# Kernel optimization log

Hardware: AMD Instinct MI355X
Metric: run time of the kernel (lower is better)

Reference implementation:

```python
import jax, jax.numpy as jnp
import numpy as np

D_MODEL = 1024
NUM_HEADS = 16
HEAD_SIZE = D_MODEL // NUM_HEADS  # 64; used ONLY as the softmax scale (module never splits heads)


def setup_inputs() -> dict:
    key = jax.random.key(0)
    ks = jax.random.split(key, 7)
    B, L, D = 4, 2048, D_MODEL
    q = jax.random.normal(ks[0], (B, L, D), dtype=jnp.float32)
    k = jax.random.normal(ks[1], (B, L, D), dtype=jnp.float32)
    v = jax.random.normal(ks[2], (B, L, D), dtype=jnp.float32)
    s = 1.0 / np.sqrt(D)
    Wq = jax.random.uniform(ks[3], (D, D), jnp.float32, -s, s)
    Wk = jax.random.uniform(ks[4], (D, D), jnp.float32, -s, s)
    Wv = jax.random.uniform(ks[5], (D, D), jnp.float32, -s, s)
    Wproj = jax.random.uniform(ks[6], (D, D), jnp.float32, -s, s)
    return {"q": q, "k": k, "v": v, "Wq": Wq, "Wk": Wk, "Wv": Wv, "Wproj": Wproj}


def reference(q, k, v, Wq, Wk, Wv, Wproj):
    # nn.Linear(x) = x @ W.T; weights stored [out, in]
    L = q.shape[1]
    qh = jnp.einsum('bld,ed->ble', q, Wq)
    kh = jnp.einsum('bld,ed->ble', k, Wk)
    vh = jnp.einsum('bld,ed->ble', v, Wv)
    # NOTE: module attends over the full d_model channel (no head split),
    # but scales by head_size ** -0.5 — faithful to the source.
    att = jnp.einsum('bqd,bkd->bqk', qh, kh) * (HEAD_SIZE ** -0.5)
    causal = jnp.tril(jnp.ones((L, L), dtype=bool))  # bias buffer
    att = jnp.where(causal, att, -jnp.inf)
    att = jax.nn.softmax(att, axis=-1)
    y = jnp.einsum('bqk,bkd->bqd', att, vh)
    y = jnp.einsum('bld,ed->ble', y, Wproj)
    return y
```

## Files before the change

### kernel.cpp

```cpp
#include <hip/hip_runtime.h>
#include <hip/hip_bf16.h>
#include <stdint.h>

typedef __bf16 bf16x8 __attribute__((ext_vector_type(8)));
typedef float  f32x4  __attribute__((ext_vector_type(4)));
typedef unsigned short ushort8v __attribute__((ext_vector_type(8)));

__device__ __forceinline__ unsigned short f2bf(float f) {
  unsigned int u = __float_as_uint(f);
  u += 0x7FFF + ((u >> 16) & 1);
  return (unsigned short)(u >> 16);
}

#define GLOAD_LDS(gptr, ldsptr)                                                     \
  __builtin_amdgcn_global_load_lds(                                                 \
      (const __attribute__((address_space(1))) unsigned int*)(gptr),                \
      (__attribute__((address_space(3))) unsigned int*)(ldsptr), 16, 0, 0)

#define BM 128
#define BN 128
#define BK 32

__global__ __launch_bounds__(256, 3) void gemm_bt(
    const unsigned short* __restrict__ A,
    const unsigned short* __restrict__ B,
    void* __restrict__ C,
    int M, int N, int K, int ntiles,
    long sAz, long sBz, long sCz,
    int mode, int tilemap, float scale)
{
  int mt, nt;
  const int orig = blockIdx.x;
  if (tilemap == 0) {
    const int nwg = gridDim.x;
    const int qq = nwg >> 3, rr = nwg & 7, xc = orig & 7, oo = orig >> 3;
    const int wg = (xc < rr ? xc * (qq + 1) : rr * (qq + 1) + (xc - rr) * qq) + oo;
    mt = wg / ntiles; nt = wg % ntiles;
  } else if (tilemap == 1) {
    mt = (int)((sqrtf(8.f * orig + 1.f) - 1.f) * 0.5f);
    int base = mt * (mt + 1) / 2;
    if (orig < base) { mt--; base = mt * (mt + 1) / 2; }
    else if (orig >= base + mt + 1) { mt++; base = mt * (mt + 1) / 2; }
    nt = orig - base;
  } else {
    const int c = orig & 15;
    mt = (c & 8) ? (15 - (c & 7)) : c;
    nt = orig >> 4;
  }
  const int z = blockIdx.y;
  const int emode = (mode == 3) ? (z == 2 ? 1 : 0) : mode;

  A += sAz * (long)z;
  B += sBz * (long)z;

  __shared__ __align__(16) unsigned short As[3][BM * BK];
  __shared__ __align__(16) unsigned short Bs[3][BN * BK];

  const int tid  = threadIdx.x;
  const int wave = tid >> 6;
  const int lane = tid & 63;
  const int wr = wave >> 1, wc = wave & 1;

  f32x4 acc[4][4];
#pragma unroll
  for (int i = 0; i < 4; ++i)
#pragma unroll
    for (int j = 0; j < 4; ++j) acc[i][j] = (f32x4){0.f, 0.f, 0.f, 0.f};

  int kiters = K / BK;
  if (tilemap == 2) { const int kl = (mt + 1) * (BM / BK); if (kl < kiters) kiters = kl; }

  const int r0 = tid >> 2, s0 = tid & 3;
  const int c0 = ((s0 ^ ((r0 >> 1) & 3)) << 3);
  const int r1 = r0 + 64;
  const int c1 = ((s0 ^ ((r1 >> 1) & 3)) << 3);
  const long aoff0 = (long)(mt * BM + r0) * K + c0;
  const long aoff1 = (long)(mt * BM + r1) * K + c1;
  const long boff0 = (long)(nt * BN + r0) * K + c0;
  const long boff1 = (long)(nt * BN + r1) * K + c1;
  const unsigned ldsw = wave * 1024;

#define STAGE(bi, k0)                                                     \
  do {                                                                    \
    GLOAD_LDS(A + aoff0 + (k0), (char*)&As[bi][0]    + ldsw);             \
    GLOAD_LDS(A + aoff1 + (k0), (char*)&As[bi][2048] + ldsw);             \
    GLOAD_LDS(B + boff0 + (k0), (char*)&Bs[bi][0]    + ldsw);             \
    GLOAD_LDS(B + boff1 + (k0), (char*)&Bs[bi][2048] + ldsw);             \
  } while (0)

  STAGE(0, 0);
  if (kiters > 1) STAGE(1, BK);

  int cur = 0;
  for (int kt = 0; kt < kiters; ++kt) {
    const int rem = kiters - 1 - kt;
    if (rem >= 2) {
      int sb = cur + 2; if (sb >= 3) sb -= 3;
      STAGE(sb, (kt + 2) * BK);
      asm volatile("s_waitcnt vmcnt(8)" ::: "memory");
    } else if (rem == 1) {
      asm volatile("s_waitcnt vmcnt(4)" ::: "memory");
    } else {
      asm volatile("s_waitcnt vmcnt(0)" ::: "memory");
    }
    __builtin_amdgcn_s_barrier();
    asm volatile("" ::: "memory");

    bf16x8 af[4], bfr[4];
#pragma unroll
    for (int i = 0; i < 4; ++i) {
      const int ar = wr * 64 + i * 16 + (lane & 15);
      const int as = ((lane >> 4) ^ ((ar >> 1) & 3)) << 3;
      af[i] = *(const bf16x8*)&As[cur][ar * BK + as];
      const int br = wc * 64 + i * 16 + (lane & 15);
      const int bs = ((lane >> 4) ^ ((br >> 1) & 3)) << 3;
      bfr[i] = *(const bf16x8*)&Bs[cur][br * BK + bs];
    }
#pragma unroll
    for (int mi = 0; mi < 4; ++mi)
#pragma unroll
      for (int ni = 0; ni < 4; ++ni)
        acc[mi][ni] = __builtin_amdgcn_mfma_f32_16x16x32_bf16(af[mi], bfr[ni], acc[mi][ni], 0, 0, 0);

    asm volatile("" ::: "memory");
    __builtin_amdgcn_s_barrier();
    cur = (cur == 2) ? 0 : cur + 1;
  }
#undef STAGE

  const int rb = mt * BM + wr * 64;
  const int cb = nt * BN + wc * 64;

  if (emode == 0) {
    unsigned short* Cb = (unsigned short*)C + sCz * (long)z;
#pragma unroll
    for (int mi = 0; mi < 4; ++mi)
#pragma unroll
      for (int ni = 0; ni < 4; ++ni) {
        const int row0 = rb + mi * 16 + ((lane >> 4) << 2);
        const int col  = cb + ni * 16 + (lane & 15);
#pragma unroll
        for (int j = 0; j < 4; ++j)
          Cb[(long)(row0 + j) * N + col] = f2bf(acc[mi][ni][j]);
      }
  } else if (emode == 1) {
    unsigned short* Cb = (unsigned short*)C + sCz * (long)z;
#pragma unroll
    for (int mi = 0; mi < 4; ++mi)
#pragma unroll
      for (int ni = 0; ni < 4; ++ni) {
        const int row0 = rb + mi * 16 + ((lane >> 4) << 2);
        const int col  = cb + ni * 16 + (lane & 15);
#pragma unroll
        for (int j = 0; j < 4; ++j) {
          const int row = row0 + j;
          const int b = row >> 11, l = row & 2047;
          Cb[((long)b * N + col) * 2048 + l] = f2bf(acc[mi][ni][j]);
        }
      }
  } else {
    float* Cf = (float*)C + sCz * (long)z;
#pragma unroll
    for (int mi = 0; mi < 4; ++mi)
#pragma unroll
      for (int ni = 0; ni < 4; ++ni) {
        const int row0 = rb + mi * 16 + ((lane >> 4) << 2);
        const int col  = cb + ni * 16 + (lane & 15);
#pragma unroll
        for (int j = 0; j < 4; ++j)
          Cf[(long)(row0 + j) * N + col] = acc[mi][ni][j] * scale;
      }
  }
}

__global__ __launch_bounds__(256) void softmax_causal(
    const float* __restrict__ S, unsigned short* __restrict__ P, int L)
{
  const int r = blockIdx.x;
  const int b = r >> 11, q = r & 2047;
  const float* srow = S + ((long)b * L + q) * L;
  unsigned short* prow = P + ((long)b * L + q) * L;
  const int len = q + 1;
  const int lenceil = ((q >> 7) + 1) << 7;
  const int tid = threadIdx.x, lane = tid & 63, wave = tid >> 6;
  const int base = tid * 8;
  const bool active = base < lenceil;
  __shared__ float red[8];

  float vv[8];
#pragma unroll
  for (int i = 0; i < 8; ++i) vv[i] = -3.4e38f;
  if (active) {
    float4 x0 = ((const float4*)srow)[tid * 2];
    float4 x1 = ((const float4*)srow)[tid * 2 + 1];
    vv[0] = x0.x; vv[1] = x0.y; vv[2] = x0.z; vv[3] = x0.w;
    vv[4] = x1.x; vv[5] = x1.y; vv[6] = x1.z; vv[7] = x1.w;
  }

  float m = -3.4e38f;
#pragma unroll
  for (int i = 0; i < 8; ++i) if (base + i < len) m = fmaxf(m, vv[i]);
#pragma unroll
  for (int o = 32; o; o >>= 1) m = fmaxf(m, __shfl_xor(m, o));
  if (lane == 0) red[wave] = m;
  __syncthreads();
  m = fmaxf(fmaxf(red[0], red[1]), fmaxf(red[2], red[3]));

  float p[8], s = 0.f;
#pragma unroll
  for (int i = 0; i < 8; ++i) {
    p[i] = (base + i < len) ? __expf(vv[i] - m) : 0.f;
    s += p[i];
  }
#pragma unroll
  for (int o = 32; o; o >>= 1) s += __shfl_xor(s, o);
  if (lane == 0) red[4 + wave] = s;
  __syncthreads();
  s = (red[4] + red[5]) + (red[6] + red[7]);
  const float inv = 1.f / s;

  if (active) {
    ushort8v o16;
#pragma unroll
    for (int i = 0; i < 8; ++i) o16[i] = f2bf(p[i] * inv);
    *(ushort8v*)(prow + base) = o16;
  }
}

__global__ __launch_bounds__(256) void convert_all(
    const float* __restrict__ q, const float* __restrict__ k, const float* __restrict__ v,
    const float* __restrict__ wq, const float* __restrict__ wk,
    const float* __restrict__ wv, const float* __restrict__ wp,
    unsigned short* __restrict__ qkv, unsigned short* __restrict__ wb)
{
  const long NQ = 8192L * 1024 / 4;
  const long NW = 1024L * 1024 / 4;
  const int blk = blockIdx.x;
  const float* src; unsigned short* dst; long n; int nb, bb;
  if (blk < 1536) {
    const int s = blk >> 9;
    src = (s == 0) ? q : (s == 1) ? k : v;
    dst = qkv + (long)s * (8192L * 1024);
    n = NQ; nb = 512; bb = blk & 511;
  } else {
    const int s = (blk - 1536) >> 6;
    src = (s == 0) ? wq : (s == 1) ? wk : (s == 2) ? wv : wp;
    dst = wb + (long)s * (1024L * 1024);
    n = NW; nb = 64; bb = (blk - 1536) & 63;
  }
  for (long i = (long)bb * 256 + threadIdx.x; i < n; i += (long)nb * 256) {
    float4 x = ((const float4*)src)[i];
    ushort4 o;
    o.x = f2bf(x.x); o.y = f2bf(x.y); o.z = f2bf(x.z); o.w = f2bf(x.w);
    ((ushort4*)dst)[i] = o;
  }
}

extern "C" void kernel_launch(void* const* d_in, const int* in_sizes, int n_in,
                              void* d_out, int out_size, void* d_ws, size_t ws_size,
                              hipStream_t stream) {
  const float* q  = (const float*)d_in[0];
  const float* k  = (const float*)d_in[1];
  const float* v  = (const float*)d_in[2];
  const float* Wq = (const float*)d_in[3];
  const float* Wk = (const float*)d_in[4];
  const float* Wv = (const float*)d_in[5];
  const float* Wp = (const float*)d_in[6];
  float* out = (float*)d_out;

  const long D  = 1024;
  const long L  = 2048;
  const long ND = 8192 * D;
  const long NS = 4L * L * L;

  char* ws = (char*)d_ws;
  unsigned short* qh    = (unsigned short*)ws;
  unsigned short* kh    = qh  + ND;
  unsigned short* vhT   = kh  + ND;
  unsigned short* P     = vhT + ND;
  unsigned short* ybf   = P   + NS;
  unsigned short* wbf   = ybf + ND;
  float*          S     = (float*)(wbf + 4L * D * D);
  unsigned short* qkvbf = (unsigned short*)S;

  convert_all<<<1792, 256, 0, stream>>>(q, k, v, Wq, Wk, Wv, Wp, qkvbf, wbf);

  gemm_bt<<<dim3(512, 3), 256, 0, stream>>>(qkvbf, wbf, qh,
      8192, 1024, 1024, 8, ND, D * D, ND, 3, 0, 1.0f);

  gemm_bt<<<dim3(136, 4), 256, 0, stream>>>(qh, kh, S,
      2048, 2048, 1024, 16, L * D, L * D, L * L, 2, 1, 0.125f);

  softmax_causal<<<8192, 256, 0, stream>>>(S, P, 2048);

  gemm_bt<<<dim3(128, 4), 256, 0, stream>>>(P, vhT, ybf,
      2048, 1024, 2048, 8, L * L, D * L, L * D, 0, 2, 1.0f);

  gemm_bt<<<dim3(512, 1), 256, 0, stream>>>(ybf, wbf + 3 * D * D, out,
      8192, 1024, 1024, 8, 0, 0, 0, 2, 0, 1.0f);
}
```

Baseline: 221.0 us.

## Fuse fp32-to-bf16 activation conversion into QKV projection and store scores as bf16

Adds a proj_fused GEMM kernel that loads fp32 q/k/v straight from global memory into registers, converts them to bf16, and writes them into swizzled LDS. This removes the separate activation conversion pass and its bf16 staging buffer, and a smaller convert_w kernel now converts only the weights. The QK^T GEMM now writes scaled scores as bf16 instead of fp32, which halves score traffic into softmax. The cost is reduced precision of pre-softmax logits, plus a register-staged A path with manual waitcnt pipelining that may stall more than direct global-to-LDS loads.

Result: no change. 223.2 us (+1.0%).

```diff
diff --git a/kernel.cpp b/kernel.cpp
--- a/kernel.cpp
+++ b/kernel.cpp
@@ -11,6 +11,9 @@
   u += 0x7FFF + ((u >> 16) & 1);
   return (unsigned short)(u >> 16);
 }
+__device__ __forceinline__ float bf2f(unsigned short h) {
+  return __uint_as_float(((unsigned int)h) << 16);
+}
 
 #define GLOAD_LDS(gptr, ldsptr)                                                     \
   __builtin_amdgcn_global_load_lds(                                                 \
@@ -20,6 +23,158 @@
 #define BM 128
 #define BN 128
 #define BK 32
+
+__global__ __launch_bounds__(256, 3) void proj_fused(
+    const float* __restrict__ Aq, const float* __restrict__ Ak, const float* __restrict__ Av,
+    const unsigned short* __restrict__ W,
+    unsigned short* __restrict__ Out)
+{
+  const int K = 1024, N = 1024;
+  const int nwg = gridDim.x, orig = blockIdx.x;
+  const int qq = nwg >> 3, rr = nwg & 7, xc = orig & 7, oo = orig >> 3;
+  const int wg = (xc < rr ? xc * (qq + 1) : rr * (qq + 1) + (xc - rr) * qq) + oo;
+  const int mt = wg >> 3, nt = wg & 7;
+  const int z = blockIdx.y;
+  const float* A = (z == 0) ? Aq : (z == 1) ? Ak : Av;
+  const unsigned short* B = W + (long)z * (1024 * 1024);
+
+  __shared__ __align__(16) unsigned short As[2][128 * 32];
+  __shared__ __align__(16) unsigned short Bs[3][128 * 32];
+
+  const int tid = threadIdx.x, wave = tid >> 6, lane = tid & 63;
+  const int wr = wave >> 1, wc = wave & 1;
+
+  f32x4 acc[4][4];
+#pragma unroll
+  for (int i = 0; i < 4; ++i)
+#pragma unroll
+    for (int j = 0; j < 4; ++j) acc[i][j] = (f32x4){0.f, 0.f, 0.f, 0.f};
+
+  const int arow = tid >> 1;
+  const int acs  = (tid & 1) * 2;
+  const int asw  = (arow >> 1) & 3;
+  const float* abase = A + (long)(mt * 128 + arow) * K + acs * 8;
+  unsigned short* wp00 = &As[0][arow * 32 + ((acs    ) ^ asw) * 8];
+  unsigned short* wp01 = &As[0][arow * 32 + ((acs + 1) ^ asw) * 8];
+  unsigned short* wp10 = &As[1][arow * 32 + ((acs    ) ^ asw) * 8];
+  unsigned short* wp11 = &As[1][arow * 32 + ((acs + 1) ^ asw) * 8];
+
+  const int r0 = tid >> 2, s0 = tid & 3;
+  const int c0 = ((s0 ^ ((r0 >> 1) & 3)) << 3);
+  const int r1 = r0 + 64;
+  const int c1 = ((s0 ^ ((r1 >> 1) & 3)) << 3);
+  const long boff0 = (long)(nt * 128 + r0) * K + c0;
+  const long boff1 = (long)(nt * 128 + r1) * K + c1;
+  const unsigned ldsw = wave * 1024;
+
+  float4 rAe0, rAe1, rAe2, rAe3, rAo0, rAo1, rAo2, rAo3;
+
+#define LOADAE(kt) do { const float4* p_ = (const float4*)(abase + (kt) * 32);      \
+    rAe0 = p_[0]; rAe1 = p_[1]; rAe2 = p_[2]; rAe3 = p_[3]; } while (0)
+#define LOADAO(kt) do { const float4* p_ = (const float4*)(abase + (kt) * 32);      \
+    rAo0 = p_[0]; rAo1 = p_[1]; rAo2 = p_[2]; rAo3 = p_[3]; } while (0)
+#define BSTAGE(m, kt) do {                                                          \
+    GLOAD_LDS(B + boff0 + (kt) * 32, (char*)&Bs[m][0]    + ldsw);                   \
+    GLOAD_LDS(B + boff1 + (kt) * 32, (char*)&Bs[m][2048] + ldsw); } while (0)
+#define CVTW(bi, a0, a1, a2, a3) do {                                               \
+    ushort8v h0_, h1_;                                                              \
+    h0_[0]=f2bf(a0.x); h0_[1]=f2bf(a0.y); h0_[2]=f2bf(a0.z); h0_[3]=f2bf(a0.w);     \
+    h0_[4]=f2bf(a1.x); h0_[5]=f2bf(a1.y); h0_[6]=f2bf(a1.z); h0_[7]=f2bf(a1.w);     \
+    h1_[0]=f2bf(a2.x); h1_[1]=f2bf(a2.y); h1_[2]=f2bf(a2.z); h1_[3]=f2bf(a2.w);     \
+    h1_[4]=f2bf(a3.x); h1_[5]=f2bf(a3.y); h1_[6]=f2bf(a3.z); h1_[7]=f2bf(a3.w);     \
+    if (bi) { *(ushort8v*)wp10 = h0_; *(ushort8v*)wp11 = h1_; }                     \
+    else    { *(ushort8v*)wp00 = h0_; *(ushort8v*)wp01 = h1_; } } while (0)
+#define COMPUTE(abuf, bmod) do {                                                    \
+    bf16x8 af_[4], bf_[4];                                                          \
+    _Pragma("unroll")                                                               \
+    for (int i_ = 0; i_ < 4; ++i_) {                                                \
+      const int ar_ = wr * 64 + i_ * 16 + (lane & 15);                              \
+      const int as_ = ((lane >> 4) ^ ((ar_ >> 1) & 3)) << 3;                        \
+      af_[i_] = *(const bf16x8*)&As[abuf][ar_ * 32 + as_];                          \
+      const int br_ = wc * 64 + i_ * 16 + (lane & 15);                              \
+      const int bs_ = ((lane >> 4) ^ ((br_ >> 1) & 3)) << 3;                        \
+      bf_[i_] = *(const bf16x8*)&Bs[bmod][br_ * 32 + bs_]; }                        \
+    _Pragma("unroll")                                                               \
+    for (int mi_ = 0; mi_ < 4; ++mi_)                                               \
+    _Pragma("unroll")                                                               \
+      for (int ni_ = 0; ni_ < 4; ++ni_)                                             \
+        acc[mi_][ni_] = __builtin_amdgcn_mfma_f32_16x16x32_bf16(                    \
+            af_[mi_], bf_[ni_], acc[mi_][ni_], 0, 0, 0); } while (0)
+
+  LOADAE(0); LOADAO(1);
+  BSTAGE(0, 0); BSTAGE(1, 1);
+  asm volatile("s_waitcnt vmcnt(2)" ::: "memory");
+  CVTW(0, rAe0, rAe1, rAe2, rAe3);
+  asm volatile("s_waitcnt lgkmcnt(0)" ::: "memory");
+  __builtin_amdgcn_s_barrier();
+  asm volatile("" ::: "memory");
+
+  int m0 = 0;
+  for (int kt = 0; kt < 30; kt += 2) {
+    const int m1 = (m0 + 1) % 3, m2 = (m0 + 2) % 3;
+    LOADAE(kt + 2);
+    BSTAGE(m2, kt + 2);
+    COMPUTE(0, m0);
+    asm volatile("s_waitcnt vmcnt(6)" ::: "memory");
+    CVTW(1, rAo0, rAo1, rAo2, rAo3);
+    asm volatile("s_waitcnt lgkmcnt(0)" ::: "memory");
+    __builtin_amdgcn_s_barrier();
+    asm volatile("" ::: "memory");
+    LOADAO(kt + 3);
+    BSTAGE(m0, kt + 3);
+    COMPUTE(1, m1);
+    asm volatile("s_waitcnt vmcnt(6)" ::: "memory");
+    CVTW(0, rAe0, rAe1, rAe2, rAe3);
+    asm volatile("s_waitcnt lgkmcnt(0)" ::: "memory");
+    __builtin_amdgcn_s_barrier();
+    asm volatile("" ::: "memory");
+    m0 = m2;
+  }
+  COMPUTE(0, 0);
+  asm volatile("s_waitcnt vmcnt(0)" ::: "memory");
+  CVTW(1, rAo0, rAo1, rAo2, rAo3);
+  asm volatile("s_waitcnt lgkmcnt(0)" ::: "memory");
+  __builtin_amdgcn_s_barrier();
+  asm volatile("" ::: "memory");
+  COMPUTE(1, 1);
+
+#undef LOADAE
+#undef LOADAO
+#undef BSTAGE
+#undef CVTW
+#undef COMPUTE
+
+  const int rb = mt * 128 + wr * 64;
+  const int cb = nt * 128 + wc * 64;
+  if (z < 2) {
+    unsigned short* Cb = Out + (long)z * (8192L * 1024);
+#pragma unroll
+    for (int mi = 0; mi < 4; ++mi)
+#pragma unroll
+      for (int ni = 0; ni < 4; ++ni) {
+        const int row0 = rb + mi * 16 + ((lane >> 4) << 2);
+        const int col  = cb + ni * 16 + (lane & 15);
+#pragma unroll
+        for (int j = 0; j < 4; ++j)
+          Cb[(long)(row0 + j) * N + col] = f2bf(acc[mi][ni][j]);
+      }
+  } else {
+    unsigned short* Cb = Out + 2L * (8192L * 1024);
+#pragma unroll
+    for (int mi = 0; mi < 4; ++mi)
+#pragma unroll
+      for (int ni = 0; ni < 4; ++ni) {
+        const int row0 = rb + mi * 16 + ((lane >> 4) << 2);
+        const int col  = cb + ni * 16 + (lane & 15);
+#pragma unroll
+        for (int j = 0; j < 4; ++j) {
+          const int row = row0 + j;
+          const int b = row >> 11, l = row & 2047;
+          Cb[((long)b * N + col) * 2048 + l] = f2bf(acc[mi][ni][j]);
+        }
+      }
+  }
+}
 
 __global__ __launch_bounds__(256, 3) void gemm_bt(
     const unsigned short* __restrict__ A,
@@ -48,7 +203,6 @@
     nt = orig >> 4;
   }
   const int z = blockIdx.y;
-  const int emode = (mode == 3) ? (z == 2 ? 1 : 0) : mode;
 
   A += sAz * (long)z;
   B += sBz * (long)z;
@@ -131,7 +285,7 @@
   const int rb = mt * BM + wr * 64;
   const int cb = nt * BN + wc * 64;
 
-  if (emode == 0) {
+  if (mode == 0) {
     unsigned short* Cb = (unsigned short*)C + sCz * (long)z;
 #pragma unroll
     for (int mi = 0; mi < 4; ++mi)
@@ -141,10 +295,10 @@
         const int col  = cb + ni * 16 + (lane & 15);
 #pragma unroll
         for (int j = 0; j < 4; ++j)
-          Cb[(long)(row0 + j) * N + col] = f2bf(acc[mi][ni][j]);
+          Cb[(long)(row0 + j) * N + col] = f2bf(acc[mi][ni][j] * scale);
       }
-  } else if (emode == 1) {
-    unsigned short* Cb = (unsigned short*)C + sCz * (long)z;
+  } else {
+    float* Cf = (float*)C + sCz * (long)z;
 #pragma unroll
     for (int mi = 0; mi < 4; ++mi)
 #pragma unroll
@@ -152,21 +306,6 @@
         const int row0 = rb + mi * 16 + ((lane >> 4) << 2);
         const int col  = cb + ni * 16 + (lane & 15);
 #pragma unroll
-        for (int j = 0; j < 4; ++j) {
-          const int row = row0 + j;
-          const int b = row >> 11, l = row & 2047;
-          Cb[((long)b * N + col) * 2048 + l] = f2bf(acc[mi][ni][j]);
-        }
-      }
-  } else {
-    float* Cf = (float*)C + sCz * (long)z;
-#pragma unroll
-    for (int mi = 0; mi < 4; ++mi)
-#pragma unroll
-      for (int ni = 0; ni < 4; ++ni) {
-        const int row0 = rb + mi * 16 + ((lane >> 4) << 2);
-        const int col  = cb + ni * 16 + (lane & 15);
-#pragma unroll
         for (int j = 0; j < 4; ++j)
           Cf[(long)(row0 + j) * N + col] = acc[mi][ni][j] * scale;
       }
@@ -174,12 +313,12 @@
 }
 
 __global__ __launch_bounds__(256) void softmax_causal(
-    const float* __restrict__ S, unsigned short* __restrict__ P, int L)
+    const unsigned short* __restrict__ S, unsigned short* __restrict__ P)
 {
   const int r = blockIdx.x;
   const int b = r >> 11, q = r & 2047;
-  const float* srow = S + ((long)b * L + q) * L;
-  unsigned short* prow = P + ((long)b * L + q) * L;
+  const unsigned short* srow = S + ((long)b * 2048 + q) * 2048;
+  unsigned short* prow = P + ((long)b * 2048 + q) * 2048;
   const int len = q + 1;
   const int lenceil = ((q >> 7) + 1) << 7;
   const int tid = threadIdx.x, lane = tid & 63, wave = tid >> 6;
@@ -191,10 +330,9 @@
 #pragma unroll
   for (int i = 0; i < 8; ++i) vv[i] = -3.4e38f;
   if (active) {
-    float4 x0 = ((const float4*)srow)[tid * 2];
-    float4 x1 = ((const float4*)srow)[tid * 2 + 1];
-    vv[0] = x0.x; vv[1] = x0.y; vv[2] = x0.z; vv[3] = x0.w;
-    vv[4] = x1.x; vv[5] = x1.y; vv[6] = x1.z; vv[7] = x1.w;
+    ushort8v xv = *(const ushort8v*)(srow + base);
+#pragma unroll
+    for (int i = 0; i < 8; ++i) vv[i] = bf2f(xv[i]);
   }
 
   float m = -3.4e38f;
@@ -227,32 +365,21 @@
   }
 }
 
-__global__ __launch_bounds__(256) void convert_all(
-    const float* __restrict__ q, const float* __restrict__ k, const float* __restrict__ v,
+__global__ __launch_bounds__(256) void convert_w(
     const float* __restrict__ wq, const float* __restrict__ wk,
     const float* __restrict__ wv, const float* __restrict__ wp,
-    unsigned short* __restrict__ qkv, unsigned short* __restrict__ wb)
+    unsigned short* __restrict__ wb)
 {
-  const long NQ = 8192L * 1024 / 4;
-  const long NW = 1024L * 1024 / 4;
-  const int blk = blockIdx.x;
-  const float* src; unsigned short* dst; long n; int nb, bb;
-  if (blk < 1536) {
-    const int s = blk >> 9;
-    src = (s == 0) ? q : (s == 1) ? k : v;
-    dst = qkv + (long)s * (8192L * 1024);
-    n = NQ; nb = 512; bb = blk & 511;
-  } else {
-    const int s = (blk - 1536) >> 6;
-    src = (s == 0) ? wq : (s == 1) ? wk : (s == 2) ? wv : wp;
-    dst = wb + (long)s * (1024L * 1024);
-    n = NW; nb = 64; bb = (blk - 1536) & 63;
-  }
-  for (long i = (long)bb * 256 + threadIdx.x; i < n; i += (long)nb * 256) {
-    float4 x = ((const float4*)src)[i];
+  const long NV = 262144;
+  for (long i = (long)blockIdx.x * 256 + threadIdx.x; i < 4 * NV;
+       i += (long)gridDim.x * 256) {
+    const int seg = (int)(i >> 18);
+    const long off = i & (NV - 1);
+    const float* src = (seg == 0) ? wq : (seg == 1) ? wk : (seg == 2) ? wv : wp;
+    float4 x = ((const float4*)src)[off];
     ushort4 o;
     o.x = f2bf(x.x); o.y = f2bf(x.y); o.z = f2bf(x.z); o.w = f2bf(x.w);
-    ((ushort4*)dst)[i] = o;
+    ((ushort4*)(wb + (long)seg * 1048576))[off] = o;
   }
 }
 
@@ -274,24 +401,22 @@
   const long NS = 4L * L * L;
 
   char* ws = (char*)d_ws;
-  unsigned short* qh    = (unsigned short*)ws;
-  unsigned short* kh    = qh  + ND;
-  unsigned short* vhT   = kh  + ND;
-  unsigned short* P     = vhT + ND;
-  unsigned short* ybf   = P   + NS;
-  unsigned short* wbf   = ybf + ND;
-  float*          S     = (float*)(wbf + 4L * D * D);
-  unsigned short* qkvbf = (unsigned short*)S;
-
-  convert_all<<<1792, 256, 0, stream>>>(q, k, v, Wq, Wk, Wv, Wp, qkvbf, wbf);
-
-  gemm_bt<<<dim3(512, 3), 256, 0, stream>>>(qkvbf, wbf, qh,
-      8192, 1024, 1024, 8, ND, D * D, ND, 3, 0, 1.0f);
+  unsigned short* qh  = (unsigned short*)ws;
+  unsigned short* kh  = qh  + ND;
+  unsigned short* vhT = kh  + ND;
+  unsigned short* P   = vhT + ND;
+  unsigned short* ybf = P   + NS;
+  unsigned short* wbf = ybf + ND;
+  unsigned short* S   = wbf + 4L * D * D;
+
+  convert_w<<<1024, 256, 0, stream>>>(Wq, Wk, Wv, Wp, wbf);
+
+  proj_fused<<<dim3(512, 3), 256, 0, stream>>>(q, k, v, wbf, qh);
 
   gemm_bt<<<dim3(136, 4), 256, 0, stream>>>(qh, kh, S,
-      2048, 2048, 1024, 16, L * D, L * D, L * L, 2, 1, 0.125f);
-
-  softmax_causal<<<8192, 256, 0, stream>>>(S, P, 2048);
+      2048, 2048, 1024, 16, L * D, L * D, L * L, 0, 1, 0.125f);
+
+  softmax_causal<<<8192, 256, 0, stream>>>(S, P);
 
   gemm_bt<<<dim3(128, 4), 256, 0, stream>>>(P, vhT, ybf,
       2048, 1024, 2048, 8, L * L, D * L, L * D, 0, 2, 1.0f);
```

## Store attention scores in bf16 and use 128x256 tiles for projection GEMMs

Applied to the files above, without the earlier changes.

The QK^T GEMM now writes scaled scores as bf16 instead of fp32, and the softmax kernel reads bf16. This halves the memory traffic of the large score matrix. A new gemm_wide kernel with 128x256 tiles and a triple-buffered LDS pipeline replaces gemm_bt for the QKV and output projections, raising reuse per block. The workspace layout is changed so that P aliases the converted-input buffer. Rounding the scores to bf16 before softmax loses some precision.

New measurement: 234.7 us. 1.06x slower.

```diff
diff --git a/kernel.cpp b/kernel.cpp
--- a/kernel.cpp
+++ b/kernel.cpp
@@ -11,11 +11,156 @@
   u += 0x7FFF + ((u >> 16) & 1);
   return (unsigned short)(u >> 16);
 }
+__device__ __forceinline__ float bf2f(unsigned short h) {
+  return __uint_as_float(((unsigned int)h) << 16);
+}
 
 #define GLOAD_LDS(gptr, ldsptr)                                                     \
   __builtin_amdgcn_global_load_lds(                                                 \
       (const __attribute__((address_space(1))) unsigned int*)(gptr),                \
       (__attribute__((address_space(3))) unsigned int*)(ldsptr), 16, 0, 0)
+
+__global__ __launch_bounds__(256, 2) void gemm_wide(
+    const unsigned short* __restrict__ A,
+    const unsigned short* __restrict__ B,
+    void* __restrict__ C,
+    int M, int N, int K, int ntiles,
+    long sAz, long sBz, long sCz,
+    int mode, float scale)
+{
+  const int nwg = gridDim.x, orig = blockIdx.x;
+  const int qq = nwg >> 3, rr = nwg & 7, xc = orig & 7, oo = orig >> 3;
+  const int wg = (xc < rr ? xc * (qq + 1) : rr * (qq + 1) + (xc - rr) * qq) + oo;
+  const int mt = wg / ntiles, nt = wg % ntiles;
+  const int z = blockIdx.y;
+  const int emode = (mode == 3) ? (z == 2 ? 1 : 0) : mode;
+
+  A += sAz * (long)z;
+  B += sBz * (long)z;
+
+  __shared__ __align__(16) unsigned short As[3][128 * 32];
+  __shared__ __align__(16) unsigned short Bs[3][256 * 32];
+
+  const int tid  = threadIdx.x;
+  const int wave = tid >> 6;
+  const int lane = tid & 63;
+  const int wr = wave >> 1, wc = wave & 1;
+
+  f32x4 acc[4][8];
+#pragma unroll
+  for (int i = 0; i < 4; ++i)
+#pragma unroll
+    for (int j = 0; j < 8; ++j) acc[i][j] = (f32x4){0.f, 0.f, 0.f, 0.f};
+
+  const int kiters = K / 32;
+
+  const int r0 = tid >> 2, s0 = tid & 3;
+  const int c0 = ((s0 ^ ((r0 >> 1) & 3)) << 3);
+  const long aoff0 = (long)(mt * 128 + r0) * K + c0;
+  const long aoff1 = (long)(mt * 128 + 64 + r0) * K + c0;
+  const long boff0 = (long)(nt * 256 + r0) * K + c0;
+  const long boff1 = (long)(nt * 256 + 64 + r0) * K + c0;
+  const long boff2 = (long)(nt * 256 + 128 + r0) * K + c0;
+  const long boff3 = (long)(nt * 256 + 192 + r0) * K + c0;
+  const unsigned ldsw = wave * 1024;
+
+#define STAGE(bi, k0)                                                     \
+  do {                                                                    \
+    GLOAD_LDS(A + aoff0 + (k0), (char*)&As[bi][0]    + ldsw);             \
+    GLOAD_LDS(A + aoff1 + (k0), (char*)&As[bi][2048] + ldsw);             \
+    GLOAD_LDS(B + boff0 + (k0), (char*)&Bs[bi][0]    + ldsw);             \
+    GLOAD_LDS(B + boff1 + (k0), (char*)&Bs[bi][2048] + ldsw);             \
+    GLOAD_LDS(B + boff2 + (k0), (char*)&Bs[bi][4096] + ldsw);             \
+    GLOAD_LDS(B + boff3 + (k0), (char*)&Bs[bi][6144] + ldsw);             \
+  } while (0)
+
+  STAGE(0, 0);
+  if (kiters > 1) STAGE(1, 32);
+
+  int cur = 0;
+  for (int kt = 0; kt < kiters; ++kt) {
+    const int rem = kiters - 1 - kt;
+    if (rem >= 2) {
+      int sb = cur + 2; if (sb >= 3) sb -= 3;
+      STAGE(sb, (kt + 2) * 32);
+      asm volatile("s_waitcnt vmcnt(12)" ::: "memory");
+    } else if (rem == 1) {
+      asm volatile("s_waitcnt vmcnt(6)" ::: "memory");
+    } else {
+      asm volatile("s_waitcnt vmcnt(0)" ::: "memory");
+    }
+    __builtin_amdgcn_s_barrier();
+    asm volatile("" ::: "memory");
+
+    bf16x8 af[4], bfr[8];
+#pragma unroll
+    for (int i = 0; i < 4; ++i) {
+      const int ar = wr * 64 + i * 16 + (lane & 15);
+      const int as = ((lane >> 4) ^ ((ar >> 1) & 3)) << 3;
+      af[i] = *(const bf16x8*)&As[cur][ar * 32 + as];
+    }
+#pragma unroll
+    for (int j = 0; j < 8; ++j) {
+      const int br = (j >> 2) * 128 + wc * 64 + (j & 3) * 16 + (lane & 15);
+      const int bs = ((lane >> 4) ^ ((br >> 1) & 3)) << 3;
+      bfr[j] = *(const bf16x8*)&Bs[cur][br * 32 + bs];
+    }
+#pragma unroll
+    for (int mi = 0; mi < 4; ++mi)
+#pragma unroll
+      for (int ni = 0; ni < 8; ++ni)
+        acc[mi][ni] = __builtin_amdgcn_mfma_f32_16x16x32_bf16(af[mi], bfr[ni], acc[mi][ni], 0, 0, 0);
+
+    asm volatile("" ::: "memory");
+    __builtin_amdgcn_s_barrier();
+    cur = (cur == 2) ? 0 : cur + 1;
+  }
+#undef STAGE
+
+  const int rb = mt * 128 + wr * 64;
+  const int cbase = nt * 256;
+
+  if (emode == 0) {
+    unsigned short* Cb = (unsigned short*)C + sCz * (long)z;
+#pragma unroll
+    for (int mi = 0; mi < 4; ++mi)
+#pragma unroll
+      for (int ni = 0; ni < 8; ++ni) {
+        const int row0 = rb + mi * 16 + ((lane >> 4) << 2);
+        const int col  = cbase + (ni >> 2) * 128 + wc * 64 + (ni & 3) * 16 + (lane & 15);
+#pragma unroll
+        for (int j = 0; j < 4; ++j)
+          Cb[(long)(row0 + j) * N + col] = f2bf(acc[mi][ni][j] * scale);
+      }
+  } else if (emode == 1) {
+    unsigned short* Cb = (unsigned short*)C + sCz * (long)z;
+#pragma unroll
+    for (int mi = 0; mi < 4; ++mi)
+#pragma unroll
+      for (int ni = 0; ni < 8; ++ni) {
+        const int row0 = rb + mi * 16 + ((lane >> 4) << 2);
+        const int col  = cbase + (ni >> 2) * 128 + wc * 64 + (ni & 3) * 16 + (lane & 15);
+#pragma unroll
+        for (int j = 0; j < 4; ++j) {
+          const int row = row0 + j;
+          const int b = row >> 11, l = row & 2047;
+          Cb[((long)b * N + col) * 2048 + l] = f2bf(acc[mi][ni][j]);
+        }
+      }
+  } else {
+    float* Cf = (float*)C + sCz * (long)z;
+#pragma unroll
+    for (int mi = 0; mi < 4; ++mi)
+#pragma unroll
+      for (int ni = 0; ni < 8; ++ni) {
+        const int row0 = rb + mi * 16 + ((lane >> 4) << 2);
+        const int col  = cbase + (ni >> 2) * 128 + wc * 64 + (ni & 3) * 16 + (lane & 15);
+#pragma unroll
+        for (int j = 0; j < 4; ++j)
+          Cf[(long)(row0 + j) * N + col] = acc[mi][ni][j] * scale;
+      }
+  }
+}
 
 #define BM 128
 #define BN 128
@@ -48,7 +193,6 @@
     nt = orig >> 4;
   }
   const int z = blockIdx.y;
-  const int emode = (mode == 3) ? (z == 2 ? 1 : 0) : mode;
 
   A += sAz * (long)z;
   B += sBz * (long)z;
@@ -131,7 +275,7 @@
   const int rb = mt * BM + wr * 64;
   const int cb = nt * BN + wc * 64;
 
-  if (emode == 0) {
+  if (mode == 0) {
     unsigned short* Cb = (unsigned short*)C + sCz * (long)z;
 #pragma unroll
     for (int mi = 0; mi < 4; ++mi)
@@ -141,10 +285,10 @@
         const int col  = cb + ni * 16 + (lane & 15);
 #pragma unroll
         for (int j = 0; j < 4; ++j)
-          Cb[(long)(row0 + j) * N + col] = f2bf(acc[mi][ni][j]);
+          Cb[(long)(row0 + j) * N + col] = f2bf(acc[mi][ni][j] * scale);
       }
-  } else if (emode == 1) {
-    unsigned short* Cb = (unsigned short*)C + sCz * (long)z;
+  } else {
+    float* Cf = (float*)C + sCz * (long)z;
 #pragma unroll
     for (int mi = 0; mi < 4; ++mi)
 #pragma unroll
@@ -152,21 +296,6 @@
         const int row0 = rb + mi * 16 + ((lane >> 4) << 2);
         const int col  = cb + ni * 16 + (lane & 15);
 #pragma unroll
-        for (int j = 0; j < 4; ++j) {
-          const int row = row0 + j;
-          const int b = row >> 11, l = row & 2047;
-          Cb[((long)b * N + col) * 2048 + l] = f2bf(acc[mi][ni][j]);
-        }
-      }
-  } else {
-    float* Cf = (float*)C + sCz * (long)z;
-#pragma unroll
-    for (int mi = 0; mi < 4; ++mi)
-#pragma unroll
-      for (int ni = 0; ni < 4; ++ni) {
-        const int row0 = rb + mi * 16 + ((lane >> 4) << 2);
-        const int col  = cb + ni * 16 + (lane & 15);
-#pragma unroll
         for (int j = 0; j < 4; ++j)
           Cf[(long)(row0 + j) * N + col] = acc[mi][ni][j] * scale;
       }
@@ -174,12 +303,12 @@
 }
 
 __global__ __launch_bounds__(256) void softmax_causal(
-    const float* __restrict__ S, unsigned short* __restrict__ P, int L)
+    const unsigned short* __restrict__ S, unsigned short* __restrict__ P)
 {
   const int r = blockIdx.x;
   const int b = r >> 11, q = r & 2047;
-  const float* srow = S + ((long)b * L + q) * L;
-  unsigned short* prow = P + ((long)b * L + q) * L;
+  const unsigned short* srow = S + ((long)b * 2048 + q) * 2048;
+  unsigned short* prow = P + ((long)b * 2048 + q) * 2048;
   const int len = q + 1;
   const int lenceil = ((q >> 7) + 1) << 7;
   const int tid = threadIdx.x, lane = tid & 63, wave = tid >> 6;
@@ -191,10 +320,9 @@
 #pragma unroll
   for (int i = 0; i < 8; ++i) vv[i] = -3.4e38f;
   if (active) {
-    float4 x0 = ((const float4*)srow)[tid * 2];
-    float4 x1 = ((const float4*)srow)[tid * 2 + 1];
-    vv[0] = x0.x; vv[1] = x0.y; vv[2] = x0.z; vv[3] = x0.w;
-    vv[4] = x1.x; vv[5] = x1.y; vv[6] = x1.z; vv[7] = x1.w;
+    ushort8v xv = *(const ushort8v*)(srow + base);
+#pragma unroll
+    for (int i = 0; i < 8; ++i) vv[i] = bf2f(xv[i]);
   }
 
   float m = -3.4e38f;
@@ -277,25 +405,25 @@
   unsigned short* qh    = (unsigned short*)ws;
   unsigned short* kh    = qh  + ND;
   unsigned short* vhT   = kh  + ND;
-  unsigned short* P     = vhT + ND;
-  unsigned short* ybf   = P   + NS;
-  unsigned short* wbf   = ybf + ND;
-  float*          S     = (float*)(wbf + 4L * D * D);
-  unsigned short* qkvbf = (unsigned short*)S;
+  unsigned short* wbf   = vhT + ND;
+  unsigned short* S     = wbf + 4L * D * D;
+  unsigned short* qkvbf = S   + NS;
+  unsigned short* P     = qkvbf;
+  unsigned short* ybf   = P + NS;
 
   convert_all<<<1792, 256, 0, stream>>>(q, k, v, Wq, Wk, Wv, Wp, qkvbf, wbf);
 
-  gemm_bt<<<dim3(512, 3), 256, 0, stream>>>(qkvbf, wbf, qh,
-      8192, 1024, 1024, 8, ND, D * D, ND, 3, 0, 1.0f);
+  gemm_wide<<<dim3(256, 3), 256, 0, stream>>>(qkvbf, wbf, qh,
+      8192, 1024, 1024, 4, ND, D * D, ND, 3, 1.0f);
 
   gemm_bt<<<dim3(136, 4), 256, 0, stream>>>(qh, kh, S,
-      2048, 2048, 1024, 16, L * D, L * D, L * L, 2, 1, 0.125f);
-
-  softmax_causal<<<8192, 256, 0, stream>>>(S, P, 2048);
+      2048, 2048, 1024, 16, L * D, L * D, L * L, 0, 1, 0.125f);
+
+  softmax_causal<<<8192, 256, 0, stream>>>(S, P);
 
   gemm_bt<<<dim3(128, 4), 256, 0, stream>>>(P, vhT, ybf,
       2048, 1024, 2048, 8, L * L, D * L, L * D, 0, 2, 1.0f);
 
-  gemm_bt<<<dim3(512, 1), 256, 0, stream>>>(ybf, wbf + 3 * D * D, out,
-      8192, 1024, 1024, 8, 0, 0, 0, 2, 0, 1.0f);
-}
+  gemm_wide<<<dim3(256, 1), 256, 0, stream>>>(ybf, wbf + 3 * D * D, out,
+      8192, 1024, 1024, 4, 0, 0, 0, 2, 1.0f);
+}
```

## Store attention scores in bf16 and switch GEMM to double-buffered LDS

Applied to the files above, without the earlier changes.

The QK^T GEMM now writes scaled scores as bf16 instead of fp32, and softmax reads them as bf16. This halves the score-matrix write and read traffic. Separately, the GEMM pipeline drops from three LDS stages to two, and launch bounds rise to allow more resident blocks per CU. Storing scores in bf16 loses precision before softmax. Shallower prefetch may expose more memory latency, traded for higher occupancy.

New measurement: 222.2 us. Within noise of the previous version (+0.5%).

```diff
diff --git a/kernel.cpp b/kernel.cpp
--- a/kernel.cpp
+++ b/kernel.cpp
@@ -11,6 +11,9 @@
   u += 0x7FFF + ((u >> 16) & 1);
   return (unsigned short)(u >> 16);
 }
+__device__ __forceinline__ float bf2f(unsigned short h) {
+  return __uint_as_float(((unsigned int)h) << 16);
+}
 
 #define GLOAD_LDS(gptr, ldsptr)                                                     \
   __builtin_amdgcn_global_load_lds(                                                 \
@@ -21,7 +24,7 @@
 #define BN 128
 #define BK 32
 
-__global__ __launch_bounds__(256, 3) void gemm_bt(
+__global__ __launch_bounds__(256, 5) void gemm_bt(
     const unsigned short* __restrict__ A,
     const unsigned short* __restrict__ B,
     void* __restrict__ C,
@@ -53,8 +56,8 @@
   A += sAz * (long)z;
   B += sBz * (long)z;
 
-  __shared__ __align__(16) unsigned short As[3][BM * BK];
-  __shared__ __align__(16) unsigned short Bs[3][BN * BK];
+  __shared__ __align__(16) unsigned short As[2][BM * BK];
+  __shared__ __align__(16) unsigned short Bs[2][BN * BK];
 
   const int tid  = threadIdx.x;
   const int wave = tid >> 6;
@@ -89,16 +92,11 @@
   } while (0)
 
   STAGE(0, 0);
-  if (kiters > 1) STAGE(1, BK);
 
   int cur = 0;
   for (int kt = 0; kt < kiters; ++kt) {
-    const int rem = kiters - 1 - kt;
-    if (rem >= 2) {
-      int sb = cur + 2; if (sb >= 3) sb -= 3;
-      STAGE(sb, (kt + 2) * BK);
-      asm volatile("s_waitcnt vmcnt(8)" ::: "memory");
-    } else if (rem == 1) {
+    if (kt + 1 < kiters) {
+      STAGE(cur ^ 1, (kt + 1) * BK);
       asm volatile("s_waitcnt vmcnt(4)" ::: "memory");
     } else {
       asm volatile("s_waitcnt vmcnt(0)" ::: "memory");
@@ -124,7 +122,7 @@
 
     asm volatile("" ::: "memory");
     __builtin_amdgcn_s_barrier();
-    cur = (cur == 2) ? 0 : cur + 1;
+    cur ^= 1;
   }
 #undef STAGE
 
@@ -141,7 +139,7 @@
         const int col  = cb + ni * 16 + (lane & 15);
 #pragma unroll
         for (int j = 0; j < 4; ++j)
-          Cb[(long)(row0 + j) * N + col] = f2bf(acc[mi][ni][j]);
+          Cb[(long)(row0 + j) * N + col] = f2bf(acc[mi][ni][j] * scale);
       }
   } else if (emode == 1) {
     unsigned short* Cb = (unsigned short*)C + sCz * (long)z;
@@ -174,12 +172,12 @@
 }
 
 __global__ __launch_bounds__(256) void softmax_causal(
-    const float* __restrict__ S, unsigned short* __restrict__ P, int L)
+    const unsigned short* __restrict__ S, unsigned short* __restrict__ P)
 {
   const int r = blockIdx.x;
   const int b = r >> 11, q = r & 2047;
-  const float* srow = S + ((long)b * L + q) * L;
-  unsigned short* prow = P + ((long)b * L + q) * L;
+  const unsigned short* srow = S + ((long)b * 2048 + q) * 2048;
+  unsigned short* prow = P + ((long)b * 2048 + q) * 2048;
   const int len = q + 1;
   const int lenceil = ((q >> 7) + 1) << 7;
   const int tid = threadIdx.x, lane = tid & 63, wave = tid >> 6;
@@ -191,10 +189,9 @@
 #pragma unroll
   for (int i = 0; i < 8; ++i) vv[i] = -3.4e38f;
   if (active) {
-    float4 x0 = ((const float4*)srow)[tid * 2];
-    float4 x1 = ((const float4*)srow)[tid * 2 + 1];
-    vv[0] = x0.x; vv[1] = x0.y; vv[2] = x0.z; vv[3] = x0.w;
-    vv[4] = x1.x; vv[5] = x1.y; vv[6] = x1.z; vv[7] = x1.w;
+    ushort8v xv = *(const ushort8v*)(srow + base);
+#pragma unroll
+    for (int i = 0; i < 8; ++i) vv[i] = bf2f(xv[i]);
   }
 
   float m = -3.4e38f;
@@ -277,11 +274,11 @@
   unsigned short* qh    = (unsigned short*)ws;
   unsigned short* kh    = qh  + ND;
   unsigned short* vhT   = kh  + ND;
-  unsigned short* P     = vhT + ND;
-  unsigned short* ybf   = P   + NS;
-  unsigned short* wbf   = ybf + ND;
-  float*          S     = (float*)(wbf + 4L * D * D);
-  unsigned short* qkvbf = (unsigned short*)S;
+  unsigned short* wbf   = vhT + ND;
+  unsigned short* S     = wbf + 4L * D * D;
+  unsigned short* qkvbf = S   + NS;
+  unsigned short* P     = qkvbf;
+  unsigned short* ybf   = P + NS;
 
   convert_all<<<1792, 256, 0, stream>>>(q, k, v, Wq, Wk, Wv, Wp, qkvbf, wbf);
 
@@ -289,9 +286,9 @@
       8192, 1024, 1024, 8, ND, D * D, ND, 3, 0, 1.0f);
 
   gemm_bt<<<dim3(136, 4), 256, 0, stream>>>(qh, kh, S,
-      2048, 2048, 1024, 16, L * D, L * D, L * L, 2, 1, 0.125f);
-
-  softmax_causal<<<8192, 256, 0, stream>>>(S, P, 2048);
+      2048, 2048, 1024, 16, L * D, L * D, L * L, 0, 1, 0.125f);
+
+  softmax_causal<<<8192, 256, 0, stream>>>(S, P);
 
   gemm_bt<<<dim3(128, 4), 256, 0, stream>>>(P, vhT, ybf,
       2048, 1024, 2048, 8, L * L, D * L, L * D, 0, 2, 1.0f);
```
